# Optimization experiments

Measured on AMD Instinct MI355X. Metric: run time of the kernel, lower is better.

The kernel has to match this reference:

```python
import jax, jax.numpy as jnp
import numpy as np

B = 4096    # batch
IN = 2048   # input_dim of mapper
N = 512     # n: dim of linear subspace (z)
K = 1024    # k: ambient dim (y)
NQ = 8      # number of quadratic constraints
M_ROWS = 2 * N  # linear inequality rows (box)


def setup_inputs() -> dict:
    key = jax.random.key(0)
    ks = jax.random.split(key, 6)
    x = jax.random.normal(ks[0], (B, IN), jnp.float32)
    # mapper: Linear(IN -> N+1)
    W_map = jax.random.normal(ks[1], (N + 1, IN), jnp.float32) / np.float32(np.sqrt(IN))
    b_map = jnp.zeros((N + 1,), jnp.float32)
    # Linear constraints in the subspace: box |z_j| <= 1, with z0 = 0 strictly feasible
    eye_n = jnp.eye(N, dtype=jnp.float32)
    A_p = jnp.concatenate([eye_n, -eye_n], axis=0)          # [2N, N]
    b_p = jnp.ones((M_ROWS, 1), jnp.float32)
    z0 = jnp.zeros((N, 1), jnp.float32)
    # D = A_p / ((b_p - A_p @ z0) @ ones(1,N))  -- row-wise slack normalization
    D = A_p / (b_p - A_p @ z0)                              # [2N, N]
    # Affine lift y = NA_E @ z + y1
    NA_E = jax.random.normal(ks[2], (K, N), jnp.float32) / np.float32(np.sqrt(N))
    y1 = 0.01 * jax.random.normal(ks[3], (K, 1), jnp.float32)
    # Quadratic constraints 0.5 y^T P y + q^T y + r <= 0, P PSD (>= 2I)
    Mrand = jax.random.normal(ks[4], (NQ, K, K), jnp.float32)
    all_P = 2.0 * (jnp.einsum('ikm,ijm->ikj', Mrand, Mrand) / K + jnp.eye(K, dtype=jnp.float32))
    all_q = jnp.zeros((NQ, K, 1), jnp.float32)
    # choose r so that y0 = NA_E@z0 + y1 is strictly interior: c = -1
    w = (NA_E @ z0 + y1)[:, 0]                              # [K]
    half_wPw = 0.5 * jnp.einsum('k,ikj,j->i', w, all_P, w)  # [NQ]
    all_r = (-(half_wPw + all_q[:, :, 0] @ w) - 1.0).reshape(NQ, 1, 1)
    return dict(x=x, W_map=W_map, b_map=b_map, D=D, NA_E=NA_E, y1=y1, z0=z0,
                all_P=all_P, all_q=all_q, all_r=all_r)


def _forward(x, W_map, b_map, D, NA_E, y1, z0, all_P, all_q, all_r):
    # mapper: input -> [B, N+1]
    qm = x @ W_map.T + b_map
    v = qm[:, :N]                                   # direction in subspace [B, N]
    beta = qm[:, N]                                 # scalar per sample [B]
    # v_bar = normalize(v) (torch F.normalize semantics, eps=1e-12)
    vn = jnp.linalg.norm(v, axis=1, keepdims=True)
    v_bar = v / jnp.maximum(vn, 1e-12)
    # kappa from linear constraints: relu(max_j (D @ v_bar)_j)
    kappa = jax.nn.relu(jnp.max(v_bar @ D.T, axis=1))        # [B]
    # kappa from quadratic constraints
    w = (NA_E @ z0 + y1)[:, 0]                      # y0 in ambient space [K]
    rho = v_bar @ NA_E.T                            # [B, K]
    Prho = jnp.einsum('ikj,bj->bik', all_P, rho)    # [B, NQ, K]
    a = 0.5 * jnp.einsum('bik,bk->bi', Prho, rho)   # [B, NQ]
    Pw_plus_q = jnp.einsum('ikj,j->ik', all_P, w) + all_q[:, :, 0]  # [NQ, K]
    bq = rho @ Pw_plus_q.T                          # [B, NQ]
    c = 0.5 * jnp.einsum('k,ikj,j->i', w, all_P, w) + all_q[:, :, 0] @ w + all_r[:, 0, 0]  # [NQ]
    disc = bq * bq - 4.0 * a * c                    # > 0 since c < 0, a > 0
    lam = (-bq + jnp.sqrt(disc)) / (2.0 * a)        # max step along v_bar per constraint
    kappa = jnp.maximum(kappa, jnp.max(1.0 / lam, axis=1))
    # walker_2: alpha = 1 / (exp(beta) + kappa)  (<= 1/kappa, guaranteed feasible)
    alpha = 1.0 / (jnp.exp(beta) + kappa)           # [B]
    z = z0[:, 0] + alpha[:, None] * v_bar           # [B, N]
    y = z @ NA_E.T + y1[:, 0]                       # getyFromz: y = NA_E z + y1, [B, K]
    return y


def reference(x, W_map, b_map, D, NA_E, y1, z0, all_P, all_q, all_r):
    return _forward(x, W_map, b_map, D, NA_E, y1, z0, all_P, all_q, all_r)
```

## Files before the change

### kernel.cpp

```cpp
#include <hip/hip_runtime.h>

#define B_ROWS 4096
#define IN_DIM 2048
#define N_DIM  512
#define K_DIM  1024
#define NQ     8

typedef __attribute__((ext_vector_type(8))) short short8;
typedef __attribute__((ext_vector_type(8))) unsigned short ushort8;
typedef __attribute__((ext_vector_type(4))) float f32x4;

constexpr size_t OFF_REGA  = 0;
constexpr size_t OFF_REGB  = 16777216;
constexpr size_t OFF_GBF   = 25165824;
constexpr size_t OFF_NAEBF = 29360128;
constexpr size_t OFF_NAETB = 30408704;
constexpr size_t OFF_WVBF  = 31457280;
constexpr size_t OFF_QMV   = 33554432;
constexpr size_t OFF_VBARB = 41943040;
constexpr size_t OFF_BETA  = 46137344;
constexpr size_t OFF_KAP   = OFF_BETA + 16384;
constexpr size_t OFF_W     = OFF_KAP  + 16384;
constexpr size_t OFF_PWQ   = OFF_W    + 4096;
constexpr size_t OFF_C     = OFF_PWQ  + 32768;
constexpr size_t OFF_ASUM  = OFF_C    + 1024;

__device__ __forceinline__ unsigned short f2bf(float f) {
    unsigned int u = __builtin_bit_cast(unsigned int, f);
    u = (u + 0x7fffu + ((u >> 16) & 1u)) >> 16;
    return (unsigned short)u;
}
__device__ __forceinline__ float bf2f(unsigned short h) {
    unsigned int u = ((unsigned int)h) << 16;
    return __builtin_bit_cast(float, u);
}
__device__ __forceinline__ void gll16(const void* g, void* l) {
    __builtin_amdgcn_global_load_lds(
        (const __attribute__((address_space(1))) unsigned int*)g,
        (__attribute__((address_space(3))) unsigned int*)l, 16, 0, 0);
}

template<int BM, int BN, int MODE>
__global__ __launch_bounds__(256)
void mfma_abt(const unsigned short* __restrict__ A,
              const unsigned short* __restrict__ Bm,
              float* __restrict__ Cf, unsigned short* __restrict__ Cb,
              int N, int Kd, int lda, int ldb,
              const float* __restrict__ bias,
              const unsigned short* __restrict__ red, int ishift,
              float* __restrict__ aout,
              long sA, long sB, long sC)
{
    constexpr int FM = BM / 32, FN = BN / 32;
    __shared__ unsigned short As[2][BM * 32];
    __shared__ unsigned short Bs[2][BN * 32];
    A  += (size_t)sA * blockIdx.z;
    Bm += (size_t)sB * blockIdx.z;
    const int tid  = threadIdx.x;
    const int lane = tid & 63, wave = tid >> 6;
    const int wm = wave >> 1, wn = wave & 1;
    const int lg = lane >> 4, lr = lane & 15;
    const int m0 = blockIdx.y * BM, n0 = blockIdx.x * BN;

    const int mask = (1 << ishift) - 1;
    int nt, diagStep;
    if constexpr (MODE == 2) {
        nt = ((n0 & mask) + BN) >> 5;
        diagStep = (n0 & mask) >> 5;
    } else {
        nt = Kd >> 5; diagStep = -1;
    }

    f32x4 acc[FM][FN] = {};

    auto STAGE = [&](int buf, int k0) {
        #pragma unroll
        for (int r = 0; r < BM / 64; ++r) {
            const int l16 = (r << 8) + tid;
            const int row = l16 >> 2;
            const int c8  = (l16 & 3) << 3;
            gll16(&A[(size_t)(m0 + row) * lda + k0 + c8], &As[buf][(size_t)l16 << 3]);
        }
        #pragma unroll
        for (int r = 0; r < BN / 64; ++r) {
            const int l16 = (r << 8) + tid;
            const int row = l16 >> 2;
            const int c8  = (l16 & 3) << 3;
            gll16(&Bm[(size_t)(n0 + row) * ldb + k0 + c8], &Bs[buf][(size_t)l16 << 3]);
        }
    };

    STAGE(0, 0);
    __syncthreads();
    int cur = 0;

    for (int t = 0; t < nt; ++t) {
        if (t + 1 < nt) STAGE(cur ^ 1, (t + 1) << 5);
        if constexpr (MODE == 2) {
            if (t == diagStep) {
                #pragma unroll
                for (int fm = 0; fm < FM; ++fm)
                    #pragma unroll
                    for (int fn = 0; fn < FN; ++fn)
                        #pragma unroll
                        for (int r = 0; r < 4; ++r)
                            acc[fm][fn][r] *= 2.0f;
            }
        }
        short8 af[FM], bfr[FN];
        #pragma unroll
        for (int f = 0; f < FM; ++f)
            af[f]  = *reinterpret_cast<const short8*>(&As[cur][(wm * (BM/2) + f * 16 + lr) * 32 + lg * 8]);
        #pragma unroll
        for (int f = 0; f < FN; ++f)
            bfr[f] = *reinterpret_cast<const short8*>(&Bs[cur][(wn * (BN/2) + f * 16 + lr) * 32 + lg * 8]);
        #pragma unroll
        for (int fm = 0; fm < FM; ++fm)
            #pragma unroll
            for (int fn = 0; fn < FN; ++fn)
                acc[fm][fn] = __builtin_amdgcn_mfma_f32_16x16x32_bf16(
                                  af[fm], bfr[fn], acc[fm][fn], 0, 0, 0);
        __syncthreads();
        cur ^= 1;
    }

    if constexpr (MODE == 0) {
        #pragma unroll
        for (int fm = 0; fm < FM; ++fm)
            #pragma unroll
            for (int r = 0; r < 4; ++r) {
                const int m = m0 + wm * (BM/2) + fm * 16 + lg * 4 + r;
                #pragma unroll
                for (int fn = 0; fn < FN; ++fn) {
                    const int n = n0 + wn * (BN/2) + fn * 16 + lr;
                    Cf[(size_t)m * N + n] = acc[fm][fn][r] + (bias ? bias[n] : 0.f);
                }
            }
    } else if constexpr (MODE == 1) {
        unsigned short* C = Cb + (size_t)sC * blockIdx.z;
        #pragma unroll
        for (int fm = 0; fm < FM; ++fm)
            #pragma unroll
            for (int r = 0; r < 4; ++r) {
                const int m = m0 + wm * (BM/2) + fm * 16 + lg * 4 + r;
                #pragma unroll
                for (int fn = 0; fn < FN; ++fn) {
                    const int n = n0 + wn * (BN/2) + fn * 16 + lr;
                    C[(size_t)m * N + n] = f2bf(acc[fm][fn][r]);
                }
            }
    } else {
        const int i = n0 >> ishift;
        #pragma unroll
        for (int fm = 0; fm < FM; ++fm)
            #pragma unroll
            for (int r = 0; r < 4; ++r) {
                const int m = m0 + wm * (BM/2) + fm * 16 + lg * 4 + r;
                float p = 0.f;
                #pragma unroll
                for (int fn = 0; fn < FN; ++fn) {
                    const int ng = (n0 & mask) + wn * (BN/2) + fn * 16 + lr;
                    p = fmaf(acc[fm][fn][r], bf2f(red[(size_t)m * (mask + 1) + ng]), p);
                }
                #pragma unroll
                for (int off = 1; off < 16; off <<= 1) p += __shfl_xor(p, off);
                if (lr == 0) atomicAdd(&aout[(size_t)m * NQ + i], p);
            }
    }
}

__global__ __launch_bounds__(256)
void kprep(const float* __restrict__ all_P, const float* __restrict__ W_map,
           const float* __restrict__ NA_E, const float* __restrict__ z0,
           const float* __restrict__ y1,
           unsigned short* __restrict__ P_bf, unsigned short* __restrict__ Wv_bf,
           unsigned short* __restrict__ nae_bf, unsigned short* __restrict__ naet_bf,
           float* __restrict__ w)
{
    int id = blockIdx.x;
    const int tid = threadIdx.x;
    const float* src = nullptr; unsigned short* dst = nullptr;
    if (id < 4096)       { src = all_P; dst = P_bf; }
    else if (id < 4608)  { id -= 4096; src = W_map; dst = Wv_bf; }
    else if (id < 4864)  { id -= 4608; src = NA_E;  dst = nae_bf; }
    if (src) {
        const size_t base = ((size_t)id * 2048) + (size_t)tid * 8;
        const float4 a = *reinterpret_cast<const float4*>(&src[base]);
        const float4 b = *reinterpret_cast<const float4*>(&src[base + 4]);
        ushort8 o;
        o[0] = f2bf(a.x); o[1] = f2bf(a.y); o[2] = f2bf(a.z); o[3] = f2bf(a.w);
        o[4] = f2bf(b.x); o[5] = f2bf(b.y); o[6] = f2bf(b.z); o[7] = f2bf(b.w);
        *reinterpret_cast<ushort8*>(&dst[base]) = o;
        return;
    }
    if (id < 5376) {
        id -= 4864;
        const int bx = id & 15, by = id >> 4;
        __shared__ float t[32][33];
        const int r = tid & 31, c = tid >> 5;
        #pragma unroll
        for (int cc = c; cc < 32; cc += 8)
            t[cc][r] = NA_E[(size_t)(by * 32 + cc) * N_DIM + bx * 32 + r];
        __syncthreads();
        #pragma unroll
        for (int cc = c; cc < 32; cc += 8)
            naet_bf[(size_t)(bx * 32 + cc) * K_DIM + by * 32 + r] = f2bf(t[r][cc]);
        return;
    }
    {
        const int k = id - 5376;
        const float* rw = NA_E + (size_t)k * N_DIM;
        float s = fmaf(rw[tid], z0[tid], rw[tid + 256] * z0[tid + 256]);
        #pragma unroll
        for (int off = 32; off; off >>= 1) s += __shfl_down(s, off);
        __shared__ float red[4];
        if ((tid & 63) == 0) red[tid >> 6] = s;
        __syncthreads();
        if (tid == 0) w[k] = red[0] + red[1] + red[2] + red[3] + y1[k];
    }
}

__global__ __launch_bounds__(256)
void kbetax(const float* __restrict__ x, const float* __restrict__ W_map,
            const float* __restrict__ b_map, float* __restrict__ beta,
            unsigned short* __restrict__ x_bf)
{
    const int b = blockIdx.x, tid = threadIdx.x;
    const float* xr = x + (size_t)b * IN_DIM;
    const float* wr = W_map + (size_t)N_DIM * IN_DIM;
    const float4 xa = *reinterpret_cast<const float4*>(&xr[tid * 8]);
    const float4 xb = *reinterpret_cast<const float4*>(&xr[tid * 8 + 4]);
    const float4 wa = *reinterpret_cast<const float4*>(&wr[tid * 8]);
    const float4 wb = *reinterpret_cast<const float4*>(&wr[tid * 8 + 4]);
    ushort8 o;
    o[0] = f2bf(xa.x); o[1] = f2bf(xa.y); o[2] = f2bf(xa.z); o[3] = f2bf(xa.w);
    o[4] = f2bf(xb.x); o[5] = f2bf(xb.y); o[6] = f2bf(xb.z); o[7] = f2bf(xb.w);
    *reinterpret_cast<ushort8*>(&x_bf[(size_t)b * IN_DIM + tid * 8]) = o;
    float s = xa.x * wa.x + xa.y * wa.y + xa.z * wa.z + xa.w * wa.w
            + xb.x * wb.x + xb.y * wb.y + xb.z * wb.z + xb.w * wb.w;
    #pragma unroll
    for (int off = 32; off; off >>= 1) s += __shfl_down(s, off);
    __shared__ float red[4];
    if ((tid & 63) == 0) red[tid >> 6] = s;
    __syncthreads();
    if (tid == 0) beta[b] = red[0] + red[1] + red[2] + red[3] + b_map[N_DIM];
}

__global__ __launch_bounds__(256)
void knorm(const float* __restrict__ qm, unsigned short* __restrict__ vbarbf,
           float* __restrict__ kap0)
{
    const int b = blockIdx.x, tid = threadIdx.x;
    const float v0 = qm[(size_t)b * N_DIM + tid];
    const float v1 = qm[(size_t)b * N_DIM + tid + 256];
    float s = fmaf(v0, v0, v1 * v1);
    #pragma unroll
    for (int off = 32; off; off >>= 1) s += __shfl_down(s, off);
    __shared__ float rs[4]; __shared__ float sden;
    if ((tid & 63) == 0) rs[tid >> 6] = s;
    __syncthreads();
    if (tid == 0) sden = fmaxf(sqrtf(rs[0] + rs[1] + rs[2] + rs[3]), 1e-12f);
    __syncthreads();
    const float b0 = v0 / sden, b1 = v1 / sden;
    vbarbf[(size_t)b * N_DIM + tid]       = f2bf(b0);
    vbarbf[(size_t)b * N_DIM + tid + 256] = f2bf(b1);
    float m = fmaxf(fabsf(b0), fabsf(b1));
    #pragma unroll
    for (int off = 32; off; off >>= 1) m = fmaxf(m, __shfl_down(m, off));
    __shared__ float rm[4];
    if ((tid & 63) == 0) rm[tid >> 6] = m;
    __syncthreads();
    if (tid == 0) kap0[b] = fmaxf(fmaxf(rm[0], rm[1]), fmaxf(rm[2], rm[3]));
}

__global__ __launch_bounds__(256)
void kpwq(const float* __restrict__ P, const float* __restrict__ q,
          const float* __restrict__ w, float* __restrict__ Pwq)
{
    const int row = blockIdx.x, tid = threadIdx.x;
    const float* Pr = P + ((size_t)row << 10);
    float s = 0.f;
    #pragma unroll
    for (int t = 0; t < 4; ++t) {
        const int j = tid + 256 * t;
        s = fmaf(Pr[j], w[j], s);
    }
    #pragma unroll
    for (int off = 32; off; off >>= 1) s += __shfl_down(s, off);
    __shared__ float red[4];
    if ((tid & 63) == 0) red[tid >> 6] = s;
    __syncthreads();
    if (tid == 0) Pwq[row] = red[0] + red[1] + red[2] + red[3] + q[row];
}

__global__ __launch_bounds__(256)
void kc(const float* __restrict__ Pwq, const float* __restrict__ q,
        const float* __restrict__ w, const float* __restrict__ rr,
        float* __restrict__ c)
{
    const int i = blockIdx.x, tid = threadIdx.x;
    float s = 0.f;
    for (int k = tid; k < K_DIM; k += 256) {
        const float wk = w[k];
        s = fmaf(wk, Pwq[i * K_DIM + k], s);
        s = fmaf(q[i * K_DIM + k], wk, s);
    }
    #pragma unroll
    for (int off = 32; off; off >>= 1) s += __shfl_down(s, off);
    __shared__ float red[4];
    if ((tid & 63) == 0) red[tid >> 6] = s;
    __syncthreads();
    if (tid == 0) c[i] = 0.5f * (red[0] + red[1] + red[2] + red[3]) + rr[i];
}

__global__ __launch_bounds__(256)
void kfinal(const float* __restrict__ rho, const float* __restrict__ asum,
            const float* __restrict__ Pwq, const float* __restrict__ c,
            const float* __restrict__ kap0, const float* __restrict__ beta,
            const float* __restrict__ w, float* __restrict__ y)
{
    const int b = blockIdx.x, tid = threadIdx.x;
    __shared__ float rsh[K_DIM];
    const float* rrow = rho + (size_t)b * K_DIM;
    #pragma unroll
    for (int t = 0; t < 4; ++t) rsh[tid + 256 * t] = rrow[tid + 256 * t];
    __syncthreads();

    __shared__ float bqsh[NQ];
    const int i = tid >> 5, lane32 = tid & 31;
    float s = 0.f;
    for (int k = lane32; k < K_DIM; k += 32)
        s = fmaf(rsh[k], Pwq[i * K_DIM + k], s);
    #pragma unroll
    for (int off = 16; off; off >>= 1) s += __shfl_xor(s, off);
    if (lane32 == 0) bqsh[i] = s;
    __syncthreads();

    __shared__ float salpha;
    if (tid == 0) {
        float kap = kap0[b];
        float invmax = -3.4e38f;
        #pragma unroll
        for (int q_ = 0; q_ < NQ; ++q_) {
            const float a    = 0.5f * asum[(size_t)b * NQ + q_];
            const float bqv  = bqsh[q_];
            const float disc = bqv * bqv - 4.f * a * c[q_];
            const float lam  = (-bqv + sqrtf(disc)) / (2.f * a);
            invmax = fmaxf(invmax, 1.f / lam);
        }
        kap = fmaxf(kap, invmax);
        salpha = 1.f / (expf(beta[b]) + kap);
    }
    __syncthreads();
    const float alpha = salpha;
    #pragma unroll
    for (int t = 0; t < 4; ++t) {
        const int k = tid + 256 * t;
        y[(size_t)b * K_DIM + k] = fmaf(alpha, rsh[k], w[k]);
    }
}

extern "C" void kernel_launch(void* const* d_in, const int* in_sizes, int n_in,
                              void* d_out, int out_size, void* d_ws, size_t ws_size,
                              hipStream_t stream)
{
    const float* x     = (const float*)d_in[0];
    const float* W_map = (const float*)d_in[1];
    const float* b_map = (const float*)d_in[2];
    const float* NA_E  = (const float*)d_in[4];
    const float* y1    = (const float*)d_in[5];
    const float* z0    = (const float*)d_in[6];
    const float* all_P = (const float*)d_in[7];
    const float* all_q = (const float*)d_in[8];
    const float* all_r = (const float*)d_in[9];
    float* y = (float*)d_out;

    char* ws = (char*)d_ws;
    unsigned short* P_bf    = (unsigned short*)(ws + OFF_REGA);
    unsigned short* x_bf    = (unsigned short*)(ws + OFF_REGA);
    float*          rho     = (float*)         (ws + OFF_REGA);
    unsigned short* Tt_bf   = (unsigned short*)(ws + OFF_REGB);
    unsigned short* G_bf    = (unsigned short*)(ws + OFF_GBF);
    unsigned short* nae_bf  = (unsigned short*)(ws + OFF_NAEBF);
    unsigned short* naet_bf = (unsigned short*)(ws + OFF_NAETB);
    unsigned short* Wv_bf   = (unsigned short*)(ws + OFF_WVBF);
    float*          qm_v    = (float*)(ws + OFF_QMV);
    unsigned short* vbar_bf = (unsigned short*)(ws + OFF_VBARB);
    float* beta = (float*)(ws + OFF_BETA);
    float* kap0 = (float*)(ws + OFF_KAP);
    float* w    = (float*)(ws + OFF_W);
    float* Pwq  = (float*)(ws + OFF_PWQ);
    float* c    = (float*)(ws + OFF_C);
    float* asum = (float*)(ws + OFF_ASUM);

    hipMemsetAsync(asum, 0, (size_t)B_ROWS * NQ * sizeof(float), stream);

    kprep<<<6400, 256, 0, stream>>>(all_P, W_map, NA_E, z0, y1,
                                    P_bf, Wv_bf, nae_bf, naet_bf, w);
    kpwq<<<NQ * K_DIM, 256, 0, stream>>>(all_P, all_q, w, Pwq);
    kc  <<<NQ, 256, 0, stream>>>(Pwq, all_q, w, all_r, c);

    mfma_abt<64, 64, 1><<<dim3(16, 8, 8), 256, 0, stream>>>(
        naet_bf, P_bf, nullptr, Tt_bf, 1024, 1024, 1024, 1024,
        nullptr, nullptr, 0, nullptr, 0, (long)K_DIM * K_DIM, (long)N_DIM * K_DIM);
    mfma_abt<64, 64, 1><<<dim3(8, 8, 8), 256, 0, stream>>>(
        naet_bf, Tt_bf, nullptr, G_bf, 512, 1024, 1024, 1024,
        nullptr, nullptr, 0, nullptr, 0, (long)N_DIM * K_DIM, (long)N_DIM * N_DIM);

    kbetax<<<B_ROWS, 256, 0, stream>>>(x, W_map, b_map, beta, x_bf);

    mfma_abt<64, 64, 0><<<dim3(8, 64), 256, 0, stream>>>(
        x_bf, Wv_bf, qm_v, nullptr, 512, 2048, 2048, 2048,
        b_map, nullptr, 0, nullptr, 0, 0, 0);
    knorm<<<B_ROWS, 256, 0, stream>>>(qm_v, vbar_bf, kap0);

    mfma_abt<64, 64, 0><<<dim3(16, 64), 256, 0, stream>>>(
        vbar_bf, nae_bf, rho, nullptr, 1024, 512, 512, 512,
        nullptr, nullptr, 0, nullptr, 0, 0, 0);

    mfma_abt<128, 128, 2><<<dim3(32, 32), 256, 0, stream>>>(
        vbar_bf, G_bf, nullptr, nullptr, 4096, 512, 512, 512,
        nullptr, vbar_bf, 9, asum, 0, 0, 0);

    kfinal<<<B_ROWS, 256, 0, stream>>>(rho, asum, Pwq, c, kap0, beta, w, y);
}
```

Before: 283.4 us.

## Widen GEMM K-tile to 64 with XOR-swizzled LDS and reorder MODE2 blocks

The templated MFMA GEMM gains a BK parameter, and every call now uses a 64-wide K tile. Global-to-LDS loads store 16-byte chunks with an XOR swizzle on the row, and the fragment reads undo it, to cut LDS bank conflicts and halve the number of barriers per K. MODE 2 blocks are remapped so the long triangular tiles are scheduled first, for better load balance. The asum memset is folded into the kprep kernel and kpwq/kc are moved later in the stream, which trades a bigger LDS footprint per block for less launch overhead.

```diff
diff --git a/kernel.cpp b/kernel.cpp
--- a/kernel.cpp
+++ b/kernel.cpp
@@ -40,7 +40,7 @@
         (__attribute__((address_space(3))) unsigned int*)l, 16, 0, 0);
 }
 
-template<int BM, int BN, int MODE>
+template<int BM, int BN, int BK, int MODE>
 __global__ __launch_bounds__(256)
 void mfma_abt(const unsigned short* __restrict__ A,
               const unsigned short* __restrict__ Bm,
@@ -52,41 +52,46 @@
               long sA, long sB, long sC)
 {
     constexpr int FM = BM / 32, FN = BN / 32;
-    __shared__ unsigned short As[2][BM * 32];
-    __shared__ unsigned short Bs[2][BN * 32];
+    constexpr int KCH = BK / 8;
+    constexpr int CA = BM * BK / 2048, CB = BN * BK / 2048;
+    __shared__ unsigned short As[2][BM * BK];
+    __shared__ unsigned short Bs[2][BN * BK];
     A  += (size_t)sA * blockIdx.z;
     Bm += (size_t)sB * blockIdx.z;
     const int tid  = threadIdx.x;
     const int lane = tid & 63, wave = tid >> 6;
     const int wm = wave >> 1, wn = wave & 1;
     const int lg = lane >> 4, lr = lane & 15;
-    const int m0 = blockIdx.y * BM, n0 = blockIdx.x * BN;
+    int nblk = blockIdx.x;
+    if constexpr (MODE == 2)
+        nblk = ((nblk & 7) << 2) | (3 - (nblk >> 3));
+    const int m0 = blockIdx.y * BM, n0 = nblk * BN;
 
     const int mask = (1 << ishift) - 1;
     int nt, diagStep;
     if constexpr (MODE == 2) {
-        nt = ((n0 & mask) + BN) >> 5;
-        diagStep = (n0 & mask) >> 5;
+        nt = ((n0 & mask) + BN) / BK;
+        diagStep = (n0 & mask) / BK;
     } else {
-        nt = Kd >> 5; diagStep = -1;
+        nt = Kd / BK; diagStep = -1;
     }
 
     f32x4 acc[FM][FN] = {};
 
     auto STAGE = [&](int buf, int k0) {
         #pragma unroll
-        for (int r = 0; r < BM / 64; ++r) {
-            const int l16 = (r << 8) + tid;
-            const int row = l16 >> 2;
-            const int c8  = (l16 & 3) << 3;
-            gll16(&A[(size_t)(m0 + row) * lda + k0 + c8], &As[buf][(size_t)l16 << 3]);
+        for (int it = 0; it < CA; ++it) {
+            const int idx = it * 256 + tid;
+            const int row = idx / KCH, ch = idx % KCH;
+            const int csrc = (ch ^ (row & 7)) << 3;
+            gll16(&A[(size_t)(m0 + row) * lda + k0 + csrc], &As[buf][idx * 8]);
         }
         #pragma unroll
-        for (int r = 0; r < BN / 64; ++r) {
-            const int l16 = (r << 8) + tid;
-            const int row = l16 >> 2;
-            const int c8  = (l16 & 3) << 3;
-            gll16(&Bm[(size_t)(n0 + row) * ldb + k0 + c8], &Bs[buf][(size_t)l16 << 3]);
+        for (int it = 0; it < CB; ++it) {
+            const int idx = it * 256 + tid;
+            const int row = idx / KCH, ch = idx % KCH;
+            const int csrc = (ch ^ (row & 7)) << 3;
+            gll16(&Bm[(size_t)(n0 + row) * ldb + k0 + csrc], &Bs[buf][idx * 8]);
         }
     };
 
@@ -95,7 +100,7 @@
     int cur = 0;
 
     for (int t = 0; t < nt; ++t) {
-        if (t + 1 < nt) STAGE(cur ^ 1, (t + 1) << 5);
+        if (t + 1 < nt) STAGE(cur ^ 1, (t + 1) * BK);
         if constexpr (MODE == 2) {
             if (t == diagStep) {
                 #pragma unroll
@@ -107,19 +112,28 @@
                             acc[fm][fn][r] *= 2.0f;
             }
         }
-        short8 af[FM], bfr[FN];
-        #pragma unroll
-        for (int f = 0; f < FM; ++f)
-            af[f]  = *reinterpret_cast<const short8*>(&As[cur][(wm * (BM/2) + f * 16 + lr) * 32 + lg * 8]);
-        #pragma unroll
-        for (int f = 0; f < FN; ++f)
-            bfr[f] = *reinterpret_cast<const short8*>(&Bs[cur][(wn * (BN/2) + f * 16 + lr) * 32 + lg * 8]);
-        #pragma unroll
-        for (int fm = 0; fm < FM; ++fm)
-            #pragma unroll
-            for (int fn = 0; fn < FN; ++fn)
-                acc[fm][fn] = __builtin_amdgcn_mfma_f32_16x16x32_bf16(
-                                  af[fm], bfr[fn], acc[fm][fn], 0, 0, 0);
+        #pragma unroll
+        for (int kk = 0; kk < BK / 32; ++kk) {
+            short8 af[FM], bfr[FN];
+            #pragma unroll
+            for (int f = 0; f < FM; ++f) {
+                const int rA = wm * (BM / 2) + f * 16 + lr;
+                af[f] = *reinterpret_cast<const short8*>(
+                    &As[cur][rA * BK + ((((kk << 2) + lg) ^ (rA & 7)) << 3)]);
+            }
+            #pragma unroll
+            for (int f = 0; f < FN; ++f) {
+                const int rB = wn * (BN / 2) + f * 16 + lr;
+                bfr[f] = *reinterpret_cast<const short8*>(
+                    &Bs[cur][rB * BK + ((((kk << 2) + lg) ^ (rB & 7)) << 3)]);
+            }
+            #pragma unroll
+            for (int fm = 0; fm < FM; ++fm)
+                #pragma unroll
+                for (int fn = 0; fn < FN; ++fn)
+                    acc[fm][fn] = __builtin_amdgcn_mfma_f32_16x16x32_bf16(
+                                      af[fm], bfr[fn], acc[fm][fn], 0, 0, 0);
+        }
         __syncthreads();
         cur ^= 1;
     }
@@ -175,7 +189,7 @@
            const float* __restrict__ y1,
            unsigned short* __restrict__ P_bf, unsigned short* __restrict__ Wv_bf,
            unsigned short* __restrict__ nae_bf, unsigned short* __restrict__ naet_bf,
-           float* __restrict__ w)
+           float* __restrict__ w, float* __restrict__ asum)
 {
     int id = blockIdx.x;
     const int tid = threadIdx.x;
@@ -207,7 +221,7 @@
             naet_bf[(size_t)(bx * 32 + cc) * K_DIM + by * 32 + r] = f2bf(t[r][cc]);
         return;
     }
-    {
+    if (id < 6400) {
         const int k = id - 5376;
         const float* rw = NA_E + (size_t)k * N_DIM;
         float s = fmaf(rw[tid], z0[tid], rw[tid + 256] * z0[tid + 256]);
@@ -217,6 +231,13 @@
         if ((tid & 63) == 0) red[tid >> 6] = s;
         __syncthreads();
         if (tid == 0) w[k] = red[0] + red[1] + red[2] + red[3] + y1[k];
+        return;
+    }
+    {
+        const size_t base = ((size_t)(id - 6400) * 2048) + (size_t)tid * 8;
+        float4 z = make_float4(0.f, 0.f, 0.f, 0.f);
+        *reinterpret_cast<float4*>(&asum[base]) = z;
+        *reinterpret_cast<float4*>(&asum[base + 4]) = z;
     }
 }
 
@@ -393,34 +414,33 @@
     float* c    = (float*)(ws + OFF_C);
     float* asum = (float*)(ws + OFF_ASUM);
 
-    hipMemsetAsync(asum, 0, (size_t)B_ROWS * NQ * sizeof(float), stream);
-
-    kprep<<<6400, 256, 0, stream>>>(all_P, W_map, NA_E, z0, y1,
-                                    P_bf, Wv_bf, nae_bf, naet_bf, w);
-    kpwq<<<NQ * K_DIM, 256, 0, stream>>>(all_P, all_q, w, Pwq);
-    kc  <<<NQ, 256, 0, stream>>>(Pwq, all_q, w, all_r, c);
-
-    mfma_abt<64, 64, 1><<<dim3(16, 8, 8), 256, 0, stream>>>(
+    kprep<<<6416, 256, 0, stream>>>(all_P, W_map, NA_E, z0, y1,
+                                    P_bf, Wv_bf, nae_bf, naet_bf, w, asum);
+
+    mfma_abt<64, 64, 64, 1><<<dim3(16, 8, 8), 256, 0, stream>>>(
         naet_bf, P_bf, nullptr, Tt_bf, 1024, 1024, 1024, 1024,
         nullptr, nullptr, 0, nullptr, 0, (long)K_DIM * K_DIM, (long)N_DIM * K_DIM);
-    mfma_abt<64, 64, 1><<<dim3(8, 8, 8), 256, 0, stream>>>(
+    mfma_abt<64, 64, 64, 1><<<dim3(8, 8, 8), 256, 0, stream>>>(
         naet_bf, Tt_bf, nullptr, G_bf, 512, 1024, 1024, 1024,
         nullptr, nullptr, 0, nullptr, 0, (long)N_DIM * K_DIM, (long)N_DIM * N_DIM);
 
     kbetax<<<B_ROWS, 256, 0, stream>>>(x, W_map, b_map, beta, x_bf);
 
-    mfma_abt<64, 64, 0><<<dim3(8, 64), 256, 0, stream>>>(
+    mfma_abt<64, 64, 64, 0><<<dim3(8, 64), 256, 0, stream>>>(
         x_bf, Wv_bf, qm_v, nullptr, 512, 2048, 2048, 2048,
         b_map, nullptr, 0, nullptr, 0, 0, 0);
     knorm<<<B_ROWS, 256, 0, stream>>>(qm_v, vbar_bf, kap0);
 
-    mfma_abt<64, 64, 0><<<dim3(16, 64), 256, 0, stream>>>(
+    mfma_abt<64, 64, 64, 0><<<dim3(16, 64), 256, 0, stream>>>(
         vbar_bf, nae_bf, rho, nullptr, 1024, 512, 512, 512,
         nullptr, nullptr, 0, nullptr, 0, 0, 0);
 
-    mfma_abt<128, 128, 2><<<dim3(32, 32), 256, 0, stream>>>(
+    mfma_abt<128, 128, 64, 2><<<dim3(32, 32), 256, 0, stream>>>(
         vbar_bf, G_bf, nullptr, nullptr, 4096, 512, 512, 512,
         nullptr, vbar_bf, 9, asum, 0, 0, 0);
 
+    kpwq<<<NQ * K_DIM, 256, 0, stream>>>(all_P, all_q, w, Pwq);
+    kc  <<<NQ, 256, 0, stream>>>(Pwq, all_q, w, all_r, c);
+
     kfinal<<<B_ROWS, 256, 0, stream>>>(rho, asum, Pwq, c, kap0, beta, w, y);
 }
```

New measurement: 264.2 us. -6.8%, faster.
